# Optimization experiments

Measured on AMD Instinct MI355X. Metric: run time of the kernel, lower is better.

The kernel has to match this reference:

```python
import jax, jax.numpy as jnp
import numpy as np

B, C, H, W = 16, 512, 32, 32
G = 32  # GroupNorm groups
EPS = 1e-5


def setup_inputs() -> dict:
    key = jax.random.key(0)
    ks = jax.random.split(key, 10)
    s = 1.0 / np.sqrt(C)
    return {
        "x": jax.random.normal(ks[0], (B, C, H, W), dtype=jnp.float32),
        "Wq": jax.random.normal(ks[1], (C, C), dtype=jnp.float32) * s,
        "bq": jnp.zeros((C,), dtype=jnp.float32),
        "Wk": jax.random.normal(ks[2], (C, C), dtype=jnp.float32) * s,
        "bk": jnp.zeros((C,), dtype=jnp.float32),
        "Wv": jax.random.normal(ks[3], (C, C), dtype=jnp.float32) * s,
        "bv": jnp.zeros((C,), dtype=jnp.float32),
        "Wo": jax.random.normal(ks[4], (C, C), dtype=jnp.float32) * s,
        "bo": jnp.zeros((C,), dtype=jnp.float32),
        "gamma": jnp.ones((C,), dtype=jnp.float32),
        "beta": jnp.zeros((C,), dtype=jnp.float32),
    }


def _group_norm(x, gamma, beta):
    b, c, h, w = x.shape
    xg = x.reshape(b, G, c // G, h, w)
    mean = xg.mean(axis=(2, 3, 4), keepdims=True)
    var = xg.var(axis=(2, 3, 4), keepdims=True)
    xn = ((xg - mean) / jnp.sqrt(var + EPS)).reshape(b, c, h, w)
    return xn * gamma[None, :, None, None] + beta[None, :, None, None]


def _conv1x1(x, Wt, bias):
    # 1x1 conv == per-pixel GEMM over channels
    return jnp.einsum('oc,bchw->bohw', Wt, x) + bias[None, :, None, None]


def reference(x, Wq, bq, Wk, bk, Wv, bv, Wo, bo, gamma, beta):
    b, c, h, w = x.shape
    out = jax.nn.silu(_group_norm(x, gamma, beta))
    q = _conv1x1(out, Wq, bq)
    k = _conv1x1(out, Wk, bk)
    v = _conv1x1(out, Wv, bv)
    scale = float(c) ** (-0.5)
    # [b,h,w,H,W] attention scores over all spatial positions
    scores = jnp.einsum('bchw,bcHW->bhwHW', q, k) * scale
    attn = jax.nn.softmax(scores.reshape(b, h, w, h * w), axis=-1).reshape(b, h, w, h, w)
    hh = jnp.einsum('bhwHW,bcHW->bchw', attn, v)
    hh = _conv1x1(hh, Wo, bo)
    return hh + x
```

## Files before the change

### kernel.cpp

```cpp
#include <hip/hip_runtime.h>
#include <hip/hip_bf16.h>

#define HWN    1024
#define CCH    512
#define NBATCH 16
#define NGROUP 32
#define EPSV   1e-5f

using bf16 = __hip_bfloat16;
typedef __attribute__((ext_vector_type(4))) float f32x4;
typedef __attribute__((ext_vector_type(8))) short s16x8;

__device__ __forceinline__ float ldv(const void* p, long i, int c) {
    return c ? ((const float*)p)[i] : __bfloat162float(((const bf16*)p)[i]);
}
__device__ __forceinline__ void stv(void* p, long i, int c, float v) {
    if (c) ((float*)p)[i] = v;
    else   ((bf16*)p)[i]  = __float2bfloat16(v);
}

__device__ __forceinline__ void glds16(const void* g, void* l) {
    __builtin_amdgcn_global_load_lds(
        (const __attribute__((address_space(1))) void*)g,
        (__attribute__((address_space(3))) void*)l, 16, 0, 0);
}

__global__ __launch_bounds__(256) void detect_kernel(const void* __restrict__ x,
                                                     int* __restrict__ flag)
{
    const int tid = threadIdx.x;
    const unsigned short* h = (const unsigned short*)x;
    int ok = 0;
    for (int i = tid; i < 4096; i += 256) {
        int e = (h[2 * i] >> 7) & 0xFF;
        if (e >= 100 && e <= 135) ok++;
    }
    __shared__ int red[256];
    red[tid] = ok; __syncthreads();
    for (int off = 128; off > 0; off >>= 1) {
        if (tid < off) red[tid] += red[tid + off];
        __syncthreads();
    }
    if (tid == 0) flag[0] = (red[0] < 2458) ? 1 : 0;
}

__global__ __launch_bounds__(256) void gn_stats_kernel(const void* __restrict__ x,
                                                       const int* __restrict__ flag,
                                                       float2* __restrict__ stats)
{
    const int f = flag[0];
    const int b = blockIdx.x >> 5, g = blockIdx.x & 31;
    const long base = ((long)b * CCH + (long)g * (CCH / NGROUP)) * HWN;
    const int tid = threadIdx.x;
    const int n = (CCH / NGROUP) * HWN;
    float s = 0.f, ss = 0.f;
    if (f) {
        const float4* xp = (const float4*)((const float*)x + base);
        #pragma unroll
        for (int k = 0; k < 16; ++k) {
            float4 u = xp[tid + k * 256];
            s  += u.x + u.y + u.z + u.w;
            ss += u.x * u.x + u.y * u.y + u.z * u.z + u.w * u.w;
        }
    } else {
        for (int i = tid; i < n; i += 256) {
            float v = ldv(x, base + i, 0);
            s += v; ss += v * v;
        }
    }
    __shared__ float r1[256], r2[256];
    r1[tid] = s; r2[tid] = ss; __syncthreads();
    for (int off = 128; off > 0; off >>= 1) {
        if (tid < off) { r1[tid] += r1[tid + off]; r2[tid] += r2[tid + off]; }
        __syncthreads();
    }
    if (tid == 0) {
        float mean = r1[0] / n;
        float var  = r2[0] / n - mean * mean;
        stats[blockIdx.x] = make_float2(mean, rsqrtf(var + EPSV));
    }
}

__global__ __launch_bounds__(256)
void prep_kernel(const void* __restrict__ Wq, const void* __restrict__ Wk,
                 const void* __restrict__ Wv, const void* __restrict__ Wo,
                 const void* __restrict__ bq, const void* __restrict__ bk,
                 const void* __restrict__ bv, const void* __restrict__ bo,
                 const int* __restrict__ flag,
                 bf16* __restrict__ Wqk, bf16* __restrict__ Wvb, bf16* __restrict__ Wob,
                 float* __restrict__ bQK, float* __restrict__ bV, float* __restrict__ bO)
{
    const int f = flag[0];
    const int idx = blockIdx.x * 256 + threadIdx.x;
    if (idx < 524288) {
        const int r = idx >> 9, c = idx & 511;
        float v = (r < 512) ? ldv(Wq, (long)r * 512 + c, f)
                            : ldv(Wk, (long)(r - 512) * 512 + c, f);
        Wqk[idx] = __float2bfloat16(v);
    } else if (idx < 786432) {
        Wvb[idx - 524288] = __float2bfloat16(ldv(Wv, idx - 524288, f));
    } else if (idx < 1048576) {
        Wob[idx - 786432] = __float2bfloat16(ldv(Wo, idx - 786432, f));
    } else {
        const int j = idx - 1048576;
        if      (j < 512)  bQK[j]        = ldv(bq, j, f);
        else if (j < 1024) bQK[j]        = ldv(bk, j - 512, f);
        else if (j < 1536) bV[j - 1024]  = ldv(bv, j - 1024, f);
        else if (j < 2048) bO[j - 1536]  = ldv(bo, j - 1536, f);
    }
}

__global__ __launch_bounds__(256)
void gn_apply_kernel(const void* __restrict__ x, const int* __restrict__ flag,
                     const float2* __restrict__ stats,
                     const void* __restrict__ gamma, const void* __restrict__ beta,
                     bf16* __restrict__ xn, int zb)
{
    const int f = flag[0];
    __shared__ float t[64][65];
    const int bz = blockIdx.z;
    const int bx = zb + bz;
    const int i0 = blockIdx.x * 64;
    const int c0 = blockIdx.y * 64;
    const int tid = threadIdx.x;
    const int il = tid & 63;
    const int hq = tid >> 6;
    #pragma unroll
    for (int r = 0; r < 16; ++r) {
        const int cl = r * 4 + hq;
        const int c = c0 + cl;
        const float2 st = stats[bx * NGROUP + (c >> 4)];
        const float ga = ldv(gamma, c, f), be = ldv(beta, c, f);
        float v = ldv(x, (long)bx * CCH * HWN + (long)c * HWN + i0 + il, f);
        v = (v - st.x) * st.y * ga + be;
        t[cl][il] = v / (1.f + __expf(-v));
    }
    __syncthreads();
    #pragma unroll
    for (int r = 0; r < 16; ++r) {
        const int ii = r * 4 + hq;
        xn[(long)bz * CCH * HWN + (long)(i0 + ii) * CCH + c0 + il] =
            __float2bfloat16(t[il][ii]);
    }
}

template<bool FINAL, bool EXPS, bool RDIV>
__global__ __launch_bounds__(256)
void mfma_gemm(const bf16* __restrict__ A, const bf16* __restrict__ B,
               void* __restrict__ C, int K,
               int lda, int ldb, int ldc,
               long sA, long sB, long sC, int z0,
               const float* __restrict__ rowBias, const float* __restrict__ colBias,
               float alpha, const void* __restrict__ resid, long sR,
               const int* __restrict__ flag)
{
    __shared__ bf16 lA[2][128 * 32];
    __shared__ bf16 lB[2][128 * 32];

    const int gx = gridDim.x, gy = gridDim.y;
    const int nwg = gx * gy * (int)gridDim.z;
    const int lin = blockIdx.x + gx * (blockIdx.y + gy * blockIdx.z);
    const int qq = nwg >> 3, rr = nwg & 7;
    const int xc = lin & 7, sq = lin >> 3;
    const int nl = (xc < rr ? xc * (qq + 1) : rr * (qq + 1) + (xc - rr) * qq) + sq;
    const int bxi = nl % gx;
    const int tt  = nl / gx;
    const int byi = tt % gy;
    const int bzi = tt / gy;

    const int tid = threadIdx.x;
    const int w   = tid >> 6;
    const int l   = tid & 63;
    const int ln  = l & 15;
    const int qd  = l >> 4;
    const int wm  = (w >> 1) * 64;
    const int wn  = (w & 1) * 64;
    const int zA  = z0 + bzi;

    const bf16* Ab = A + (long)zA * sA;
    const bf16* Bb = B + (long)zA * sB;
    const int m0 = byi * 128;
    const int n0 = bxi * 128;

    const int sr   = l >> 2;
    const int kswz = ((l & 3) ^ ((l >> 3) & 3)) * 8;
    const bf16* gA0 = Ab + (long)(m0 + w * 16 + sr) * lda + kswz;
    const bf16* gA1 = gA0 + (long)64 * lda;
    const bf16* gB0 = Bb + (long)(n0 + w * 16 + sr) * ldb + kswz;
    const bf16* gB1 = gB0 + (long)64 * ldb;

    f32x4 acc[4][4];
    #pragma unroll
    for (int i = 0; i < 4; ++i)
        #pragma unroll
        for (int j = 0; j < 4; ++j)
            acc[i][j] = (f32x4){0.f, 0.f, 0.f, 0.f};

    f32x4 racc[4];
    #pragma unroll
    for (int i = 0; i < 4; ++i) racc[i] = (f32x4){0.f, 0.f, 0.f, 0.f};
    s16x8 ones;
    #pragma unroll
    for (int e = 0; e < 8; ++e) ones[e] = (short)0x3F80;

    const int swA = (qd ^ ((ln >> 1) & 3)) * 8;

    glds16(gA0, &lA[0][w * 512]);
    glds16(gA1, &lA[0][2048 + w * 512]);
    glds16(gB0, &lB[0][w * 512]);
    glds16(gB1, &lB[0][2048 + w * 512]);

    const int NK = K >> 5;
    for (int t = 0; t < NK; ++t) {
        const int p = t & 1;
        __syncthreads();
        if (t + 1 < NK) {
            const int kk = (t + 1) << 5;
            glds16(gA0 + kk, &lA[p ^ 1][w * 512]);
            glds16(gA1 + kk, &lA[p ^ 1][2048 + w * 512]);
            glds16(gB0 + kk, &lB[p ^ 1][w * 512]);
            glds16(gB1 + kk, &lB[p ^ 1][2048 + w * 512]);
        }
        s16x8 af[4], bfr[4];
        #pragma unroll
        for (int i = 0; i < 4; ++i)
            af[i] = *(const s16x8*)&lA[p][(wm + i * 16 + ln) * 32 + swA];
        #pragma unroll
        for (int j = 0; j < 4; ++j)
            bfr[j] = *(const s16x8*)&lB[p][(wn + j * 16 + ln) * 32 + swA];
        if (RDIV) {
            #pragma unroll
            for (int i = 0; i < 4; ++i)
                racc[i] = __builtin_amdgcn_mfma_f32_16x16x32_bf16(
                    af[i], ones, racc[i], 0, 0, 0);
        }
        #pragma unroll
        for (int i = 0; i < 4; ++i)
            #pragma unroll
            for (int j = 0; j < 4; ++j)
                acc[i][j] = __builtin_amdgcn_mfma_f32_16x16x32_bf16(
                    af[i], bfr[j], acc[i][j], 0, 0, 0);
    }

    const int f = (FINAL && flag) ? flag[0] : 0;
    #pragma unroll
    for (int i = 0; i < 4; ++i) {
        #pragma unroll
        for (int r = 0; r < 4; ++r) {
            const int m = m0 + wm + i * 16 + qd * 4 + r;
            const float rb = rowBias ? rowBias[m] : 0.f;
            const float inv = RDIV ? (1.f / racc[i][r]) : 1.f;
            #pragma unroll
            for (int j = 0; j < 4; ++j) {
                const int n = n0 + wn + j * 16 + ln;
                float v = alpha * acc[i][j][r] + rb;
                if (colBias) v += colBias[n];
                if (EXPS) v = __expf(fminf(v, 60.f));
                if (RDIV) v *= inv;
                const long idx = (long)zA * sC + (long)m * ldc + n;
                if (FINAL) {
                    if (resid) v += ldv(resid, (long)zA * sR + (long)m * ldc + n, f);
                    stv(C, idx, f, v);
                } else {
                    ((bf16*)C)[idx] = __float2bfloat16(v);
                }
            }
        }
    }
}

extern "C" void kernel_launch(void* const* d_in, const int* in_sizes, int n_in,
                              void* d_out, int out_size, void* d_ws, size_t ws_size,
                              hipStream_t stream)
{
    const long NX = (long)NBATCH * CCH * HWN;
    int ix, iWq, ibq, iWk, ibk, iWv, ibv, iWo, ibo, iga, ibe;
    if (in_sizes[0] == NX) {
        ix = 0; iWq = 1; ibq = 2; iWk = 3; ibk = 4; iWv = 5; ibv = 6;
        iWo = 7; ibo = 8; iga = 9; ibe = 10;
    } else {
        iWk = 0; iWo = 1; iWq = 2; iWv = 3; ibe = 4; ibk = 5; ibo = 6;
        ibq = 7; ibv = 8; iga = 9; ix = 10;
    }
    const void* x     = d_in[ix];
    const void* Wq    = d_in[iWq];
    const void* bq    = d_in[ibq];
    const void* Wk    = d_in[iWk];
    const void* bk    = d_in[ibk];
    const void* Wv    = d_in[iWv];
    const void* bv    = d_in[ibv];
    const void* Wo    = d_in[iWo];
    const void* bo    = d_in[ibo];
    const void* gamma = d_in[iga];
    const void* beta  = d_in[ibe];

    const long CHW = (long)CCH * HWN;
    const long NN  = (long)HWN * HWN;
    const size_t MB = 1ull << 20;
    char* ws = (char*)d_ws;

    bf16*   Wqk   = (bf16*)ws;
    bf16*   Wvb   = (bf16*)(ws + MB);
    bf16*   Wob   = (bf16*)(ws + MB + MB / 2);
    float*  bQK   = (float*)(ws + 2 * MB);
    float*  bV    = (float*)(ws + 2 * MB + 4096);
    float*  bO    = (float*)(ws + 2 * MB + 6144);
    float2* stats = (float2*)(ws + 2 * MB + 8192);
    int*    flag  = (int*)(ws + 2 * MB + 12288);

    dim3 blk(256);
    const float scale = 0.044194173824159216f;
    const float* FNUL = nullptr;
    const void*  VNUL = nullptr;

    detect_kernel<<<dim3(1), blk, 0, stream>>>(x, flag);
    gn_stats_kernel<<<dim3(NBATCH * NGROUP), blk, 0, stream>>>(x, flag, stats);
    prep_kernel<<<dim3(4104), blk, 0, stream>>>(Wq, Wk, Wv, Wo, bq, bk, bv, bo,
                                                flag, Wqk, Wvb, Wob, bQK, bV, bO);

    const int tier = (ws_size >= 100 * MB) ? 1 : (ws_size >= 70 * MB) ? 2 : 3;

    if (tier <= 2) {
        bf16* xn = (bf16*)(ws + 3 * MB);
        bf16* V  = (bf16*)(ws + 19 * MB);
        bf16* QK = (bf16*)(ws + 35 * MB);
        bf16* S  = (bf16*)(ws + 67 * MB);
        bf16* O  = xn;

        gn_apply_kernel<<<dim3(16, 8, NBATCH), blk, 0, stream>>>(
            x, flag, stats, gamma, beta, xn, 0);

        mfma_gemm<false, false, false><<<dim3(8, 8, NBATCH), blk, 0, stream>>>(
            xn, Wqk, QK, 512, 512, 512, 1024, CHW, 0L, NN, 0,
            FNUL, bQK, 1.f, VNUL, 0L, nullptr);
        mfma_gemm<false, false, false><<<dim3(8, 4, NBATCH), blk, 0, stream>>>(
            Wvb, xn, V, 512, 512, 512, 1024, 0L, CHW, CHW, 0,
            bV, FNUL, 1.f, VNUL, 0L, nullptr);

        if (tier == 1) {
            mfma_gemm<false, true, false><<<dim3(8, 8, NBATCH), blk, 0, stream>>>(
                QK, QK + 512, S, 512, 1024, 1024, 1024, NN, NN, NN, 0,
                FNUL, FNUL, scale, VNUL, 0L, nullptr);
            mfma_gemm<false, false, true><<<dim3(4, 8, NBATCH), blk, 0, stream>>>(
                S, V, O, 1024, 1024, 1024, 512, NN, CHW, CHW, 0,
                FNUL, FNUL, 1.f, VNUL, 0L, nullptr);
        } else {
            for (int b = 0; b < NBATCH; ++b) {
                mfma_gemm<false, true, false><<<dim3(8, 8, 1), blk, 0, stream>>>(
                    QK, QK + 512, S, 512, 1024, 1024, 1024, NN, NN, 0L, b,
                    FNUL, FNUL, scale, VNUL, 0L, nullptr);
                mfma_gemm<false, false, true><<<dim3(4, 8, 1), blk, 0, stream>>>(
                    S, V, O, 1024, 1024, 1024, 512, 0L, CHW, CHW, b,
                    FNUL, FNUL, 1.f, VNUL, 0L, nullptr);
            }
        }
        mfma_gemm<true, false, false><<<dim3(8, 4, NBATCH), blk, 0, stream>>>(
            Wob, O, d_out, 512, 512, 512, 1024, 0L, CHW, CHW, 0,
            bO, FNUL, 1.f, x, CHW, flag);
    } else {
        bf16* xn = (bf16*)(ws + 3 * MB);
        bf16* V  = (bf16*)(ws + 4 * MB);
        bf16* QK = (bf16*)(ws + 5 * MB);
        bf16* S  = (bf16*)(ws + 7 * MB);
        bf16* O  = xn;
        for (int b = 0; b < NBATCH; ++b) {
            gn_apply_kernel<<<dim3(16, 8, 1), blk, 0, stream>>>(
                x, flag, stats, gamma, beta, xn, b);
            mfma_gemm<false, false, false><<<dim3(8, 8, 1), blk, 0, stream>>>(
                xn, Wqk, QK, 512, 512, 512, 1024, 0L, 0L, 0L, 0,
                FNUL, bQK, 1.f, VNUL, 0L, nullptr);
            mfma_gemm<false, false, false><<<dim3(8, 4, 1), blk, 0, stream>>>(
                Wvb, xn, V, 512, 512, 512, 1024, 0L, 0L, 0L, 0,
                bV, FNUL, 1.f, VNUL, 0L, nullptr);
            mfma_gemm<false, true, false><<<dim3(8, 8, 1), blk, 0, stream>>>(
                QK, QK + 512, S, 512, 1024, 1024, 1024, 0L, 0L, 0L, b,
                FNUL, FNUL, scale, VNUL, 0L, nullptr);
            mfma_gemm<false, false, true><<<dim3(4, 8, 1), blk, 0, stream>>>(
                S, V, O, 1024, 1024, 1024, 512, 0L, 0L, 0L, b,
                FNUL, FNUL, 1.f, VNUL, 0L, nullptr);
            mfma_gemm<true, false, false><<<dim3(8, 4, 1), blk, 0, stream>>>(
                Wob, O, d_out, 512, 512, 512, 1024, 0L, 0L, CHW, b,
                bO, FNUL, 1.f, x, CHW, flag);
        }
    }
}
```

Baseline: 275.9 us.

## Fold Q/K/V/O weights algebraically to shrink per-pixel GEMMs in attention

Rewrites the attention algebra so scores are computed as xn·(WqᵀWk)·xnᵀ, with rank-1 bias terms handled by row and column bias vectors. The output projection is folded into V as W2 = Wo·Wv, which removes the separate Q/K projection, the V projection and the Wo GEMM. Softmax normalization moves to a column divide inside the final GEMM, using an extra MFMA against a ones vector. In exchange it adds small weight-product kernels and changes the rounding order, since the merged weights are stored in bf16.

```diff
diff --git a/kernel.cpp b/kernel.cpp
--- a/kernel.cpp
+++ b/kernel.cpp
@@ -17,6 +17,9 @@
 __device__ __forceinline__ void stv(void* p, long i, int c, float v) {
     if (c) ((float*)p)[i] = v;
     else   ((bf16*)p)[i]  = __float2bfloat16(v);
+}
+__device__ __forceinline__ float b2f(short s) {
+    return __uint_as_float(((unsigned)(unsigned short)s) << 16);
 }
 
 __device__ __forceinline__ void glds16(const void* g, void* l) {
@@ -107,6 +110,91 @@
         else if (j < 1024) bQK[j]        = ldv(bk, j - 512, f);
         else if (j < 1536) bV[j - 1024]  = ldv(bv, j - 1024, f);
         else if (j < 2048) bO[j - 1536]  = ldv(bo, j - 1536, f);
+    }
+}
+
+__global__ __launch_bounds__(256)
+void prep_t_kernel(const void* __restrict__ Wq, const void* __restrict__ Wk,
+                   const void* __restrict__ Wv, const void* __restrict__ Wo,
+                   const void* __restrict__ bq, const void* __restrict__ bk,
+                   const void* __restrict__ bv, const void* __restrict__ bo,
+                   const int* __restrict__ flag,
+                   bf16* __restrict__ WkT, bf16* __restrict__ WqT,
+                   bf16* __restrict__ WvT, bf16* __restrict__ Wob,
+                   float* __restrict__ bqf, float* __restrict__ bkf,
+                   float* __restrict__ bvf, float* __restrict__ bof)
+{
+    const int f = flag[0];
+    const int bx = blockIdx.x;
+    const int tid = threadIdx.x;
+    if (bx < 192) {
+        const int mat = bx >> 6;
+        const void* src = mat == 0 ? Wq : mat == 1 ? Wk : Wv;
+        bf16* dst = mat == 0 ? WqT : mat == 1 ? WkT : WvT;
+        const int tile = bx & 63;
+        const int r0 = (tile >> 3) * 64, c0 = (tile & 7) * 64;
+        __shared__ float t[64][65];
+        const int il = tid & 63, hq = tid >> 6;
+        #pragma unroll
+        for (int rr = 0; rr < 16; ++rr) {
+            const int r = rr * 4 + hq;
+            t[r][il] = ldv(src, (long)(r0 + r) * 512 + c0 + il, f);
+        }
+        __syncthreads();
+        #pragma unroll
+        for (int rr = 0; rr < 16; ++rr) {
+            const int cc = rr * 4 + hq;
+            dst[(long)(c0 + cc) * 512 + r0 + il] = __float2bfloat16(t[il][cc]);
+        }
+    } else if (bx < 200) {
+        const int base = (bx - 192) * 32768;
+        for (int i = tid; i < 32768; i += 256)
+            Wob[base + i] = __float2bfloat16(ldv(Wo, base + i, f));
+    } else {
+        for (int i = tid; i < 512; i += 256) {
+            bqf[i] = ldv(bq, i, f);
+            bkf[i] = ldv(bk, i, f);
+            bvf[i] = ldv(bv, i, f);
+            bof[i] = ldv(bo, i, f);
+        }
+    }
+}
+
+__global__ __launch_bounds__(256)
+void micro_kernel(const bf16* __restrict__ WkT, const bf16* __restrict__ WqT,
+                  const bf16* __restrict__ Wob,
+                  const float* __restrict__ bqf, const float* __restrict__ bkf,
+                  const float* __restrict__ bvf, const float* __restrict__ bof,
+                  float* __restrict__ w1, float* __restrict__ w2,
+                  float* __restrict__ b2, float* __restrict__ c0)
+{
+    const int bx = blockIdx.x, tid = threadIdx.x;
+    if (bx < 6) {
+        __shared__ float vec[512];
+        const float* bsrc = bx < 2 ? bqf : bx < 4 ? bkf : bvf;
+        const bf16* msrc  = bx < 2 ? WkT : bx < 4 ? WqT : Wob;
+        for (int i = tid; i < 512; i += 256) vec[i] = bsrc[i];
+        __syncthreads();
+        const int o = (bx & 1) * 256 + tid;
+        const bf16* row = msrc + (long)o * 512;
+        float s = 0.f;
+        for (int k = 0; k < 512; k += 8) {
+            s16x8 v = *(const s16x8*)&row[k];
+            #pragma unroll
+            for (int e = 0; e < 8; ++e) s += b2f(v[e]) * vec[k + e];
+        }
+        if (bx < 2)      w1[o] = s;
+        else if (bx < 4) w2[o] = s;
+        else             b2[o] = s + bof[o];
+    } else {
+        __shared__ float red[256];
+        red[tid] = bqf[tid] * bkf[tid] + bqf[tid + 256] * bkf[tid + 256];
+        __syncthreads();
+        for (int off = 128; off > 0; off >>= 1) {
+            if (tid < off) red[tid] += red[tid + off];
+            __syncthreads();
+        }
+        if (tid == 0) c0[0] = red[0];
     }
 }
 
@@ -144,13 +232,45 @@
     }
 }
 
-template<bool FINAL, bool EXPS, bool RDIV>
+__global__ __launch_bounds__(256)
+void uv_kernel(const bf16* __restrict__ xn, const float* __restrict__ w1,
+               const float* __restrict__ w2, const float* __restrict__ c0p,
+               float* __restrict__ rowB, float* __restrict__ colB, float scale)
+{
+    __shared__ float l1[512], l2[512];
+    const int tid = threadIdx.x;
+    for (int i = tid; i < 512; i += 256) { l1[i] = w1[i]; l2[i] = w2[i]; }
+    __syncthreads();
+    const float c0 = c0p[0];
+    const int row = blockIdx.x * 64 + (tid >> 2);
+    const int p   = (tid & 3) * 128;
+    const bf16* xr = xn + (long)row * 512 + p;
+    float su = 0.f, sv = 0.f;
+    for (int k = 0; k < 128; k += 8) {
+        s16x8 v = *(const s16x8*)&xr[k];
+        #pragma unroll
+        for (int e = 0; e < 8; ++e) {
+            const float xv = b2f(v[e]);
+            su += xv * l1[p + k + e];
+            sv += xv * l2[p + k + e];
+        }
+    }
+    su += __shfl_xor(su, 1); su += __shfl_xor(su, 2);
+    sv += __shfl_xor(sv, 1); sv += __shfl_xor(sv, 2);
+    if ((tid & 3) == 0) {
+        rowB[row] = scale * sv;
+        colB[row] = scale * (su + c0);
+    }
+}
+
+template<bool FINAL, bool EXPS, bool RDIV, bool RDIVB>
 __global__ __launch_bounds__(256)
 void mfma_gemm(const bf16* __restrict__ A, const bf16* __restrict__ B,
                void* __restrict__ C, int K,
                int lda, int ldb, int ldc,
                long sA, long sB, long sC, int z0,
-               const float* __restrict__ rowBias, const float* __restrict__ colBias,
+               const float* __restrict__ rowBias, long rbZ,
+               const float* __restrict__ colBias, long cbZ,
                float alpha, const void* __restrict__ resid, long sR,
                const int* __restrict__ flag)
 {
@@ -234,6 +354,12 @@
                 racc[i] = __builtin_amdgcn_mfma_f32_16x16x32_bf16(
                     af[i], ones, racc[i], 0, 0, 0);
         }
+        if (RDIVB) {
+            #pragma unroll
+            for (int j = 0; j < 4; ++j)
+                racc[j] = __builtin_amdgcn_mfma_f32_16x16x32_bf16(
+                    ones, bfr[j], racc[j], 0, 0, 0);
+        }
         #pragma unroll
         for (int i = 0; i < 4; ++i)
             #pragma unroll
@@ -242,21 +368,28 @@
                     af[i], bfr[j], acc[i][j], 0, 0, 0);
     }
 
+    float invb[4];
+    if (RDIVB) {
+        #pragma unroll
+        for (int j = 0; j < 4; ++j) invb[j] = 1.f / racc[j][0];
+    }
+
     const int f = (FINAL && flag) ? flag[0] : 0;
     #pragma unroll
     for (int i = 0; i < 4; ++i) {
         #pragma unroll
         for (int r = 0; r < 4; ++r) {
             const int m = m0 + wm + i * 16 + qd * 4 + r;
-            const float rb = rowBias ? rowBias[m] : 0.f;
+            const float rb = rowBias ? rowBias[(long)zA * rbZ + m] : 0.f;
             const float inv = RDIV ? (1.f / racc[i][r]) : 1.f;
             #pragma unroll
             for (int j = 0; j < 4; ++j) {
                 const int n = n0 + wn + j * 16 + ln;
                 float v = alpha * acc[i][j][r] + rb;
-                if (colBias) v += colBias[n];
+                if (colBias) v += colBias[(long)zA * cbZ + n];
                 if (EXPS) v = __expf(fminf(v, 60.f));
                 if (RDIV) v *= inv;
+                if (RDIVB) v *= invb[j];
                 const long idx = (long)zA * sC + (long)m * ldc + n;
                 if (FINAL) {
                     if (resid) v += ldv(resid, (long)zA * sR + (long)m * ldc + n, f);
@@ -297,90 +430,100 @@
     const long CHW = (long)CCH * HWN;
     const long NN  = (long)HWN * HWN;
     const size_t MB = 1ull << 20;
+    const size_t KB = 1024;
     char* ws = (char*)d_ws;
-
-    bf16*   Wqk   = (bf16*)ws;
-    bf16*   Wvb   = (bf16*)(ws + MB);
-    bf16*   Wob   = (bf16*)(ws + MB + MB / 2);
-    float*  bQK   = (float*)(ws + 2 * MB);
-    float*  bV    = (float*)(ws + 2 * MB + 4096);
-    float*  bO    = (float*)(ws + 2 * MB + 6144);
-    float2* stats = (float2*)(ws + 2 * MB + 8192);
-    int*    flag  = (int*)(ws + 2 * MB + 12288);
 
     dim3 blk(256);
     const float scale = 0.044194173824159216f;
     const float* FNUL = nullptr;
     const void*  VNUL = nullptr;
 
-    detect_kernel<<<dim3(1), blk, 0, stream>>>(x, flag);
-    gn_stats_kernel<<<dim3(NBATCH * NGROUP), blk, 0, stream>>>(x, flag, stats);
-    prep_kernel<<<dim3(4104), blk, 0, stream>>>(Wq, Wk, Wv, Wo, bq, bk, bv, bo,
-                                                flag, Wqk, Wvb, Wob, bQK, bV, bO);
-
-    const int tier = (ws_size >= 100 * MB) ? 1 : (ws_size >= 70 * MB) ? 2 : 3;
-
-    if (tier <= 2) {
-        bf16* xn = (bf16*)(ws + 3 * MB);
-        bf16* V  = (bf16*)(ws + 19 * MB);
-        bf16* QK = (bf16*)(ws + 35 * MB);
-        bf16* S  = (bf16*)(ws + 67 * MB);
-        bf16* O  = xn;
-
+    if (ws_size >= 88 * MB) {
+        bf16* WkT = (bf16*)ws;
+        bf16* Wob = (bf16*)(ws + 512 * KB);
+        bf16* WqT = (bf16*)(ws + MB);
+        bf16* WvT = (bf16*)(ws + MB + 512 * KB);
+        bf16* Mt  = (bf16*)(ws + 2 * MB);
+        bf16* W2  = (bf16*)(ws + 2 * MB + 512 * KB);
+        float*  bqf  = (float*)(ws + 3 * MB);
+        float*  bkf  = (float*)(ws + 3 * MB + 2 * KB);
+        float*  bvf  = (float*)(ws + 3 * MB + 4 * KB);
+        float*  bof  = (float*)(ws + 3 * MB + 6 * KB);
+        float*  w1   = (float*)(ws + 3 * MB + 8 * KB);
+        float*  w2   = (float*)(ws + 3 * MB + 10 * KB);
+        float*  b2   = (float*)(ws + 3 * MB + 12 * KB);
+        float*  c0   = (float*)(ws + 3 * MB + 14 * KB);
+        float2* stats= (float2*)(ws + 3 * MB + 16 * KB);
+        int*    flag = (int*)(ws + 3 * MB + 20 * KB);
+        float*  rowB = (float*)(ws + 3 * MB + 24 * KB);
+        float*  colB = (float*)(ws + 3 * MB + 88 * KB);
+        bf16* xn = (bf16*)(ws + 4 * MB);
+        bf16* y  = (bf16*)(ws + 20 * MB);
+        bf16* Zt = (bf16*)(ws + 36 * MB);
+        bf16* S  = (bf16*)(ws + 52 * MB);
+
+        detect_kernel<<<dim3(1), blk, 0, stream>>>(x, flag);
+        gn_stats_kernel<<<dim3(NBATCH * NGROUP), blk, 0, stream>>>(x, flag, stats);
+        prep_t_kernel<<<dim3(201), blk, 0, stream>>>(Wq, Wk, Wv, Wo, bq, bk, bv, bo,
+                                                     flag, WkT, WqT, WvT, Wob,
+                                                     bqf, bkf, bvf, bof);
+        micro_kernel<<<dim3(7), blk, 0, stream>>>(WkT, WqT, Wob, bqf, bkf, bvf, bof,
+                                                  w1, w2, b2, c0);
+        mfma_gemm<false, false, false, false><<<dim3(4, 4, 2), blk, 0, stream>>>(
+            WkT, WqT, Mt, 512, 512, 512, 512, 262144L, 262144L, 262144L, 0,
+            FNUL, 0L, FNUL, 0L, 1.f, VNUL, 0L, nullptr);
         gn_apply_kernel<<<dim3(16, 8, NBATCH), blk, 0, stream>>>(
             x, flag, stats, gamma, beta, xn, 0);
-
-        mfma_gemm<false, false, false><<<dim3(8, 8, NBATCH), blk, 0, stream>>>(
-            xn, Wqk, QK, 512, 512, 512, 1024, CHW, 0L, NN, 0,
-            FNUL, bQK, 1.f, VNUL, 0L, nullptr);
-        mfma_gemm<false, false, false><<<dim3(8, 4, NBATCH), blk, 0, stream>>>(
-            Wvb, xn, V, 512, 512, 512, 1024, 0L, CHW, CHW, 0,
-            bV, FNUL, 1.f, VNUL, 0L, nullptr);
-
-        if (tier == 1) {
-            mfma_gemm<false, true, false><<<dim3(8, 8, NBATCH), blk, 0, stream>>>(
-                QK, QK + 512, S, 512, 1024, 1024, 1024, NN, NN, NN, 0,
-                FNUL, FNUL, scale, VNUL, 0L, nullptr);
-            mfma_gemm<false, false, true><<<dim3(4, 8, NBATCH), blk, 0, stream>>>(
-                S, V, O, 1024, 1024, 1024, 512, NN, CHW, CHW, 0,
-                FNUL, FNUL, 1.f, VNUL, 0L, nullptr);
-        } else {
-            for (int b = 0; b < NBATCH; ++b) {
-                mfma_gemm<false, true, false><<<dim3(8, 8, 1), blk, 0, stream>>>(
-                    QK, QK + 512, S, 512, 1024, 1024, 1024, NN, NN, 0L, b,
-                    FNUL, FNUL, scale, VNUL, 0L, nullptr);
-                mfma_gemm<false, false, true><<<dim3(4, 8, 1), blk, 0, stream>>>(
-                    S, V, O, 1024, 1024, 1024, 512, 0L, CHW, CHW, b,
-                    FNUL, FNUL, 1.f, VNUL, 0L, nullptr);
-            }
-        }
-        mfma_gemm<true, false, false><<<dim3(8, 4, NBATCH), blk, 0, stream>>>(
-            Wob, O, d_out, 512, 512, 512, 1024, 0L, CHW, CHW, 0,
-            bO, FNUL, 1.f, x, CHW, flag);
+        uv_kernel<<<dim3(256), blk, 0, stream>>>(xn, w1, w2, c0, rowB, colB, scale);
+        mfma_gemm<false, false, false, false><<<dim3(4, 128, 1), blk, 0, stream>>>(
+            xn, Mt, y, 512, 512, 512, 512, 0L, 0L, 0L, 0,
+            FNUL, 0L, FNUL, 0L, 1.f, VNUL, 0L, nullptr);
+        mfma_gemm<false, false, false, false><<<dim3(8, 4, NBATCH), blk, 0, stream>>>(
+            W2, xn, Zt, 512, 512, 512, 1024, 0L, CHW, CHW, 0,
+            b2, 0L, FNUL, 0L, 1.f, VNUL, 0L, nullptr);
+        mfma_gemm<false, true, false, false><<<dim3(8, 8, NBATCH), blk, 0, stream>>>(
+            y, xn, S, 512, 512, 512, 1024, CHW, CHW, NN, 0,
+            rowB, 1024L, colB, 1024L, scale, VNUL, 0L, nullptr);
+        mfma_gemm<true, false, false, true><<<dim3(8, 4, NBATCH), blk, 0, stream>>>(
+            Zt, S, d_out, 1024, 1024, 1024, 1024, CHW, NN, CHW, 0,
+            FNUL, 0L, FNUL, 0L, 1.f, x, CHW, flag);
     } else {
+        bf16*   Wqk   = (bf16*)ws;
+        bf16*   Wvb   = (bf16*)(ws + MB);
+        bf16*   Wob   = (bf16*)(ws + MB + MB / 2);
+        float*  bQK   = (float*)(ws + 2 * MB);
+        float*  bV    = (float*)(ws + 2 * MB + 4096);
+        float*  bO    = (float*)(ws + 2 * MB + 6144);
+        float2* stats = (float2*)(ws + 2 * MB + 8192);
+        int*    flag  = (int*)(ws + 2 * MB + 12288);
         bf16* xn = (bf16*)(ws + 3 * MB);
         bf16* V  = (bf16*)(ws + 4 * MB);
         bf16* QK = (bf16*)(ws + 5 * MB);
         bf16* S  = (bf16*)(ws + 7 * MB);
         bf16* O  = xn;
+
+        detect_kernel<<<dim3(1), blk, 0, stream>>>(x, flag);
+        gn_stats_kernel<<<dim3(NBATCH * NGROUP), blk, 0, stream>>>(x, flag, stats);
+        prep_kernel<<<dim3(4104), blk, 0, stream>>>(Wq, Wk, Wv, Wo, bq, bk, bv, bo,
+                                                    flag, Wqk, Wvb, Wob, bQK, bV, bO);
         for (int b = 0; b < NBATCH; ++b) {
             gn_apply_kernel<<<dim3(16, 8, 1), blk, 0, stream>>>(
                 x, flag, stats, gamma, beta, xn, b);
-            mfma_gemm<false, false, false><<<dim3(8, 8, 1), blk, 0, stream>>>(
+            mfma_gemm<false, false, false, false><<<dim3(8, 8, 1), blk, 0, stream>>>(
                 xn, Wqk, QK, 512, 512, 512, 1024, 0L, 0L, 0L, 0,
-                FNUL, bQK, 1.f, VNUL, 0L, nullptr);
-            mfma_gemm<false, false, false><<<dim3(8, 4, 1), blk, 0, stream>>>(
+                FNUL, 0L, bQK, 0L, 1.f, VNUL, 0L, nullptr);
+            mfma_gemm<false, false, false, false><<<dim3(8, 4, 1), blk, 0, stream>>>(
                 Wvb, xn, V, 512, 512, 512, 1024, 0L, 0L, 0L, 0,
-                bV, FNUL, 1.f, VNUL, 0L, nullptr);
-            mfma_gemm<false, true, false><<<dim3(8, 8, 1), blk, 0, stream>>>(
+                bV, 0L, FNUL, 0L, 1.f, VNUL, 0L, nullptr);
+            mfma_gemm<false, true, false, false><<<dim3(8, 8, 1), blk, 0, stream>>>(
                 QK, QK + 512, S, 512, 1024, 1024, 1024, 0L, 0L, 0L, b,
-                FNUL, FNUL, scale, VNUL, 0L, nullptr);
-            mfma_gemm<false, false, true><<<dim3(4, 8, 1), blk, 0, stream>>>(
+                FNUL, 0L, FNUL, 0L, scale, VNUL, 0L, nullptr);
+            mfma_gemm<false, false, true, false><<<dim3(4, 8, 1), blk, 0, stream>>>(
                 S, V, O, 1024, 1024, 1024, 512, 0L, 0L, 0L, b,
-                FNUL, FNUL, 1.f, VNUL, 0L, nullptr);
-            mfma_gemm<true, false, false><<<dim3(8, 4, 1), blk, 0, stream>>>(
+                FNUL, 0L, FNUL, 0L, 1.f, VNUL, 0L, nullptr);
+            mfma_gemm<true, false, false, false><<<dim3(8, 4, 1), blk, 0, stream>>>(
                 Wob, O, d_out, 512, 512, 512, 1024, 0L, 0L, CHW, b,
-                bO, FNUL, 1.f, x, CHW, flag);
-        }
-    }
-}
+                bO, 0L, FNUL, 0L, 1.f, x, CHW, flag);
+        }
+    }
+}
```

Result: slower. 309.6 us (+12.2%).
